# Kernel tuning notes

Measured on AMD Instinct MI355X. Metric: run time of the kernel, lower is better.

Reference implementation:

```python
import jax, jax.numpy as jnp
import numpy as np

CIN = 128
COUT = 128
B = 8192
N_DIAG = 17
LENS = [9 - abs(i - 8) for i in range(N_DIAG)]  # [1,2,...,9,...,2,1]


def setup_inputs() -> dict:
    key = jax.random.key(0)
    ks = jax.random.split(key, 2 + N_DIAG)
    d = {
        "weights": jax.random.normal(ks[0], (N_DIAG, COUT, CIN), jnp.float32),
        "bias": jax.random.normal(ks[1], (N_DIAG, COUT), jnp.float32),
    }
    for i, L in enumerate(LENS):
        d[f"x{i}"] = jax.random.normal(ks[2 + i], (B, L, CIN), jnp.float32)
    return d


def _diag_idx(i):
    # board positions (r, c) on anti-diagonal r + c == i of a 9x9 board
    rs = np.arange(max(0, i - 8), min(8, i) + 1)
    cs = i - rs
    return rs, cs


def _forward(weights, bias, xs):
    b = xs[0].shape[0]
    out = jnp.zeros((b, 9, 9, weights.shape[1]), xs[0].dtype)
    for i, x in enumerate(xs):
        # per-diagonal linear transform: (B, L_i, Cin) @ (Cout, Cin)^T + bias
        y = jnp.einsum('blc,oc->blo', x, weights[i]) + bias[i]
        rs, cs = _diag_idx(i)  # static numpy indices -> jit-friendly scatter
        out = out.at[:, rs, cs, :].set(y)
    return out


def reference(weights, bias, x0, x1, x2, x3, x4, x5, x6, x7, x8, x9, x10, x11,
              x12, x13, x14, x15, x16):
    xs = (x0, x1, x2, x3, x4, x5, x6, x7, x8, x9, x10, x11, x12, x13, x14,
          x15, x16)
    return _forward(weights, bias, xs)
```

## Files before the change

### kernel.cpp

```cpp
#include <hip/hip_runtime.h>
#include <hip/hip_bf16.h>

typedef __attribute__((ext_vector_type(8))) short short8;
typedef __attribute__((ext_vector_type(4))) float f32x4;
typedef __attribute__((ext_vector_type(4))) unsigned int u32x4;

struct XPtrs { const float* p[17]; };
struct Bases { int v[18]; };

#define CPB 8

__device__ __forceinline__ unsigned short f2bf(float f) {
  unsigned u = __float_as_uint(f);
  return (unsigned short)((u + 0x7fffu + ((u >> 16) & 1u)) >> 16);
}

__global__ __launch_bounds__(1024) void convert_w_kernel(
    const float* __restrict__ W, unsigned short* __restrict__ ws) {
  const int tid = blockIdx.x * 1024 + threadIdx.x;
  const int d  = tid >> 11;
  const int s2 = tid & 2047;
  const int sg = s2 >> 7;
  const int n  = s2 & 127;
  const float* src = W + ((size_t)d * 128 + n) * 128 + sg * 8;
  float4 a = *(const float4*)(src);
  float4 b = *(const float4*)(src + 4);
  unsigned u0 = (unsigned)f2bf(a.x) | ((unsigned)f2bf(a.y) << 16);
  unsigned u1 = (unsigned)f2bf(a.z) | ((unsigned)f2bf(a.w) << 16);
  unsigned u2 = (unsigned)f2bf(b.x) | ((unsigned)f2bf(b.y) << 16);
  unsigned u3 = (unsigned)f2bf(b.z) | ((unsigned)f2bf(b.w) << 16);
  *(uint4*)(ws + (size_t)tid * 8) = make_uint4(u0, u1, u2, u3);
}

__device__ __forceinline__ unsigned pack_bf2(float lo, float hi) {
  unsigned rl = __float_as_uint(lo) + 0x8000u;
  unsigned rh = __float_as_uint(hi) + 0x8000u;
  return __builtin_amdgcn_perm(rh, rl, 0x07060302u);
}

__device__ __forceinline__ void issue_unit_loads(
    const float* __restrict__ x, int u, int wave, int lr, int lg,
    float4 (&pf)[8]) {
  const float* xr = x + ((size_t)(u * 64 + wave * 16 + lr)) * 128 + lg * 8;
#pragma unroll
  for (int s = 0; s < 4; ++s) {
    pf[2 * s]     = *(const float4*)(xr + s * 32);
    pf[2 * s + 1] = *(const float4*)(xr + s * 32 + 4);
  }
}

__device__ __forceinline__ void convert_unit(const float4 (&pf)[8],
                                             short8 (&xf)[4]) {
#pragma unroll
  for (int s = 0; s < 4; ++s) {
    float4 a0 = pf[2 * s], a1 = pf[2 * s + 1];
    u32x4 w;
    w.x = pack_bf2(a0.x, a0.y);
    w.y = pack_bf2(a0.z, a0.w);
    w.z = pack_bf2(a1.x, a1.y);
    w.w = pack_bf2(a1.z, a1.w);
    xf[s] = __builtin_bit_cast(short8, w);
  }
}

__global__ __launch_bounds__(256) void diag_linear_kernel(
    XPtrs xp, Bases bb, const unsigned short* __restrict__ wsrc,
    const float* __restrict__ bias, float* __restrict__ out) {
  const int bid = blockIdx.x;
  int d = 0;
#pragma unroll
  for (int i = 1; i < 17; ++i) d += (bid >= bb.v[i]) ? 1 : 0;
  const int L = 9 - ((d < 8) ? (8 - d) : (d - 8));
  const int start = (d > 8) ? (d - 8) : 0;
  const float* __restrict__ x = xp.p[d];
  const int u0 = (bid - bb.v[d]) * CPB;

  const int t = threadIdx.x;
  const int lane = t & 63;
  const int wave = t >> 6;
  const int lr = lane & 15;
  const int lg = lane >> 4;

  __shared__ unsigned short wlds[2048 * 8];
  __shared__ float blds[128];

  {
    const unsigned short* gw = wsrc + (size_t)d * 16384;
    typedef const __attribute__((address_space(1))) unsigned int* gas_u32;
    typedef __attribute__((address_space(3))) unsigned int* las_u32;
#pragma unroll
    for (int r = 0; r < 8; ++r) {
      const int slotbase = (wave * 8 + r) * 64;
      __builtin_amdgcn_global_load_lds(
          (gas_u32)(const void*)(gw + (size_t)(slotbase + lane) * 8),
          (las_u32)(void*)(wlds + (size_t)slotbase * 8),
          16, 0, 0);
    }
    if (t < 32) {
      __builtin_amdgcn_global_load_lds(
          (gas_u32)(const void*)(bias + d * 128 + t * 4),
          (las_u32)(void*)(blds), 16, 0, 0);
    }
  }

  float4 pA[8], pB[8];
  issue_unit_loads(x, u0,     wave, lr, lg, pA);
  issue_unit_loads(x, u0 + 1, wave, lr, lg, pB);

  __syncthreads();

  const int npair = CPB / 2;
#pragma unroll
  for (int k = 0; k < npair; ++k) {
#pragma unroll
    for (int ph = 0; ph < 2; ++ph) {
      const int u = u0 + 2 * k + ph;

      short8 xf[4];
      if (ph == 0) convert_unit(pA, xf);
      else         convert_unit(pB, xf);

      if (k + 1 < npair) {
        if (ph == 0) issue_unit_loads(x, u + 2, wave, lr, lg, pA);
        else         issue_unit_loads(x, u + 2, wave, lr, lg, pB);
      }

      f32x4 acc[8];
#pragma unroll
      for (int nb = 0; nb < 8; ++nb)
        acc[nb] = *(const f32x4*)&blds[nb * 16 + lg * 4];

#pragma unroll
      for (int s = 0; s < 4; ++s) {
#pragma unroll
        for (int nb = 0; nb < 8; ++nb) {
          short8 wf = *(const short8*)
              &wlds[(size_t)((s * 4 + lg) * 128 + nb * 16 + lr) * 8];
          acc[nb] = __builtin_amdgcn_mfma_f32_16x16x32_bf16(wf, xf[s], acc[nb], 0, 0, 0);
        }
      }

      const int f = u * 64 + wave * 16 + lr;
      const unsigned b = (unsigned)f / (unsigned)L;
      const int l = f - (int)b * L;
      float* orow = out + (size_t)b * 10368 + (size_t)(start * 8 + d) * 128
                    + (size_t)l * 1024 + lg * 4;
#pragma unroll
      for (int nb = 0; nb < 8; ++nb)
        *(f32x4*)(orow + nb * 16) = acc[nb];
    }
  }
}

extern "C" void kernel_launch(void* const* d_in, const int* in_sizes, int n_in,
                              void* d_out, int out_size, void* d_ws, size_t ws_size,
                              hipStream_t stream) {
  const float* W = (const float*)d_in[0];
  const float* bias = (const float*)d_in[1];
  XPtrs xp;
  for (int i = 0; i < 17; ++i) xp.p[i] = (const float*)d_in[2 + i];
  float* out = (float*)d_out;
  unsigned short* ws = (unsigned short*)d_ws;

  Bases bb;
  int base = 0;
  for (int i = 0; i < 17; ++i) {
    bb.v[i] = base;
    int L = 9 - ((i < 8) ? (8 - i) : (i - 8));
    base += (128 * L) / CPB;
  }
  bb.v[17] = base;

  convert_w_kernel<<<34, 1024, 0, stream>>>(W, ws);
  diag_linear_kernel<<<base, 256, 0, stream>>>(xp, bb, ws, bias, out);
}
```

Measured before the change: 161.1 us.

## Fuse weight bf16 conversion into main kernel and single-buffer x prefetch

Removes the separate weight-conversion kernel launch. Each block now loads its diagonal's fp32 weights itself, rounds them to bf16 with round-to-nearest-even and writes them to LDS. The main loop changes from a double-buffered, fully unrolled pair loop to a single-buffered loop that is not unrolled. That cuts register pressure but exposes more load latency. Every block now redundantly reads 64KB of fp32 weights instead of 32KB of bf16, with a synchronous load path before the barrier.

```diff
diff --git a/kernel.cpp b/kernel.cpp
--- a/kernel.cpp
+++ b/kernel.cpp
@@ -10,26 +10,12 @@
 
 #define CPB 8
 
-__device__ __forceinline__ unsigned short f2bf(float f) {
-  unsigned u = __float_as_uint(f);
-  return (unsigned short)((u + 0x7fffu + ((u >> 16) & 1u)) >> 16);
-}
-
-__global__ __launch_bounds__(1024) void convert_w_kernel(
-    const float* __restrict__ W, unsigned short* __restrict__ ws) {
-  const int tid = blockIdx.x * 1024 + threadIdx.x;
-  const int d  = tid >> 11;
-  const int s2 = tid & 2047;
-  const int sg = s2 >> 7;
-  const int n  = s2 & 127;
-  const float* src = W + ((size_t)d * 128 + n) * 128 + sg * 8;
-  float4 a = *(const float4*)(src);
-  float4 b = *(const float4*)(src + 4);
-  unsigned u0 = (unsigned)f2bf(a.x) | ((unsigned)f2bf(a.y) << 16);
-  unsigned u1 = (unsigned)f2bf(a.z) | ((unsigned)f2bf(a.w) << 16);
-  unsigned u2 = (unsigned)f2bf(b.x) | ((unsigned)f2bf(b.y) << 16);
-  unsigned u3 = (unsigned)f2bf(b.z) | ((unsigned)f2bf(b.w) << 16);
-  *(uint4*)(ws + (size_t)tid * 8) = make_uint4(u0, u1, u2, u3);
+__device__ __forceinline__ unsigned pack_bf2_rne(float lo, float hi) {
+  unsigned ul = __float_as_uint(lo);
+  unsigned uh = __float_as_uint(hi);
+  ul += 0x7fffu + ((ul >> 16) & 1u);
+  uh += 0x7fffu + ((uh >> 16) & 1u);
+  return __builtin_amdgcn_perm(uh, ul, 0x07060302u);
 }
 
 __device__ __forceinline__ unsigned pack_bf2(float lo, float hi) {
@@ -64,7 +50,7 @@
 }
 
 __global__ __launch_bounds__(256) void diag_linear_kernel(
-    XPtrs xp, Bases bb, const unsigned short* __restrict__ wsrc,
+    XPtrs xp, Bases bb, const float* __restrict__ W,
     const float* __restrict__ bias, float* __restrict__ out) {
   const int bid = blockIdx.x;
   int d = 0;
@@ -85,70 +71,68 @@
   __shared__ float blds[128];
 
   {
-    const unsigned short* gw = wsrc + (size_t)d * 16384;
-    typedef const __attribute__((address_space(1))) unsigned int* gas_u32;
-    typedef __attribute__((address_space(3))) unsigned int* las_u32;
+    const int n = t & 127;
+    const int kh = t >> 7;
+    const float* wrow = W + (size_t)d * 16384 + (size_t)n * 128 + kh * 64;
 #pragma unroll
-    for (int r = 0; r < 8; ++r) {
-      const int slotbase = (wave * 8 + r) * 64;
-      __builtin_amdgcn_global_load_lds(
-          (gas_u32)(const void*)(gw + (size_t)(slotbase + lane) * 8),
-          (las_u32)(void*)(wlds + (size_t)slotbase * 8),
-          16, 0, 0);
+    for (int itw = 0; itw < 8; ++itw) {
+      float4 a = *(const float4*)(wrow + itw * 8);
+      float4 b = *(const float4*)(wrow + itw * 8 + 4);
+      u32x4 v;
+      v.x = pack_bf2_rne(a.x, a.y);
+      v.y = pack_bf2_rne(a.z, a.w);
+      v.z = pack_bf2_rne(b.x, b.y);
+      v.w = pack_bf2_rne(b.z, b.w);
+      const int slot = (kh * 8 + itw) * 128 + n;
+      *(u32x4*)&wlds[(size_t)slot * 8] = v;
     }
     if (t < 32) {
+      typedef const __attribute__((address_space(1))) unsigned int* gas_u32;
+      typedef __attribute__((address_space(3))) unsigned int* las_u32;
       __builtin_amdgcn_global_load_lds(
           (gas_u32)(const void*)(bias + d * 128 + t * 4),
           (las_u32)(void*)(blds), 16, 0, 0);
     }
   }
 
-  float4 pA[8], pB[8];
-  issue_unit_loads(x, u0,     wave, lr, lg, pA);
-  issue_unit_loads(x, u0 + 1, wave, lr, lg, pB);
+  float4 pf[8];
+  issue_unit_loads(x, u0, wave, lr, lg, pf);
 
   __syncthreads();
 
-  const int npair = CPB / 2;
+#pragma unroll 1
+  for (int it = 0; it < CPB; ++it) {
+    const int u = u0 + it;
+
+    short8 xf[4];
+    convert_unit(pf, xf);
+
+    if (it + 1 < CPB)
+      issue_unit_loads(x, u + 1, wave, lr, lg, pf);
+
+    f32x4 acc[8];
 #pragma unroll
-  for (int k = 0; k < npair; ++k) {
-#pragma unroll
-    for (int ph = 0; ph < 2; ++ph) {
-      const int u = u0 + 2 * k + ph;
-
-      short8 xf[4];
-      if (ph == 0) convert_unit(pA, xf);
-      else         convert_unit(pB, xf);
-
-      if (k + 1 < npair) {
-        if (ph == 0) issue_unit_loads(x, u + 2, wave, lr, lg, pA);
-        else         issue_unit_loads(x, u + 2, wave, lr, lg, pB);
-      }
-
-      f32x4 acc[8];
-#pragma unroll
-      for (int nb = 0; nb < 8; ++nb)
-        acc[nb] = *(const f32x4*)&blds[nb * 16 + lg * 4];
+    for (int nb = 0; nb < 8; ++nb)
+      acc[nb] = *(const f32x4*)&blds[nb * 16 + lg * 4];
 
 #pragma unroll
-      for (int s = 0; s < 4; ++s) {
+    for (int s = 0; s < 4; ++s) {
 #pragma unroll
-        for (int nb = 0; nb < 8; ++nb) {
-          short8 wf = *(const short8*)
-              &wlds[(size_t)((s * 4 + lg) * 128 + nb * 16 + lr) * 8];
-          acc[nb] = __builtin_amdgcn_mfma_f32_16x16x32_bf16(wf, xf[s], acc[nb], 0, 0, 0);
-        }
+      for (int nb = 0; nb < 8; ++nb) {
+        short8 wf = *(const short8*)
+            &wlds[(size_t)((s * 4 + lg) * 128 + nb * 16 + lr) * 8];
+        acc[nb] = __builtin_amdgcn_mfma_f32_16x16x32_bf16(wf, xf[s], acc[nb], 0, 0, 0);
       }
+    }
 
-      const int f = u * 64 + wave * 16 + lr;
-      const unsigned b = (unsigned)f / (unsigned)L;
-      const int l = f - (int)b * L;
-      float* orow = out + (size_t)b * 10368 + (size_t)(start * 8 + d) * 128
-                    + (size_t)l * 1024 + lg * 4;
+    const int f = u * 64 + wave * 16 + lr;
+    const unsigned b = (unsigned)f / (unsigned)L;
+    const int l = f - (int)b * L;
+    float* orow = out + (size_t)b * 10368 + (size_t)(start * 8 + d) * 128
+                  + (size_t)l * 1024 + lg * 4;
 #pragma unroll
-      for (int nb = 0; nb < 8; ++nb)
-        *(f32x4*)(orow + nb * 16) = acc[nb];
-    }
+    for (int nb = 0; nb < 8; ++nb)
+      *(f32x4*)(orow + nb * 16) = acc[nb];
   }
 }
 
@@ -160,17 +144,15 @@
   XPtrs xp;
   for (int i = 0; i < 17; ++i) xp.p[i] = (const float*)d_in[2 + i];
   float* out = (float*)d_out;
-  unsigned short* ws = (unsigned short*)d_ws;
 
   Bases bb;
   int base = 0;
   for (int i = 0; i < 17; ++i) {
     bb.v[i] = base;
     int L = 9 - ((i < 8) ? (8 - i) : (i - 8));
-    base += (128 * L) / CPB;
+    base += 16 * L;
   }
   bb.v[17] = base;
 
-  convert_w_kernel<<<34, 1024, 0, stream>>>(W, ws);
-  diag_linear_kernel<<<base, 256, 0, stream>>>(xp, bb, ws, bias, out);
+  diag_linear_kernel<<<base, 256, 0, stream>>>(xp, bb, W, bias, out);
 }
```

After: 163.7 us. Within noise of the previous version (+1.6%).

## Halve units per block, reorder MFMA loop per output block, stop unrolling

Applied to the files above, without the earlier changes.

Cuts the units each block processes from 8 to 4, which doubles the grid size. The inner compute is reordered so each 16-column output block runs its 4 chained MFMAs and is stored right away. This drops the eight live accumulator vectors to one, lowering register pressure and raising occupancy. In exchange the MFMAs are now serially dependent, there are more per-block weight loads into LDS, and the outer loop is no longer unrolled.

```diff
diff --git a/kernel.cpp b/kernel.cpp
--- a/kernel.cpp
+++ b/kernel.cpp
@@ -8,7 +8,7 @@
 struct XPtrs { const float* p[17]; };
 struct Bases { int v[18]; };
 
-#define CPB 8
+#define CPB 4
 
 __device__ __forceinline__ unsigned short f2bf(float f) {
   unsigned u = __float_as_uint(f);
@@ -63,6 +63,28 @@
   }
 }
 
+__device__ __forceinline__ void compute_store_unit(
+    const short8 (&xf)[4], const unsigned short* __restrict__ wlds,
+    const float* __restrict__ blds, int u, int wave, int lr, int lg,
+    int L, int start, int d, float* __restrict__ out) {
+  const int f = u * 64 + wave * 16 + lr;
+  const unsigned b = (unsigned)f / (unsigned)L;
+  const int l = f - (int)b * L;
+  float* orow = out + (size_t)b * 10368 + (size_t)(start * 8 + d) * 128
+                + (size_t)l * 1024 + lg * 4;
+#pragma unroll
+  for (int nb = 0; nb < 8; ++nb) {
+    f32x4 acc = *(const f32x4*)&blds[nb * 16 + lg * 4];
+#pragma unroll
+    for (int s = 0; s < 4; ++s) {
+      short8 wf = *(const short8*)
+          &wlds[(size_t)((s * 4 + lg) * 128 + nb * 16 + lr) * 8];
+      acc = __builtin_amdgcn_mfma_f32_16x16x32_bf16(wf, xf[s], acc, 0, 0, 0);
+    }
+    *(f32x4*)(orow + nb * 16) = acc;
+  }
+}
+
 __global__ __launch_bounds__(256) void diag_linear_kernel(
     XPtrs xp, Bases bb, const unsigned short* __restrict__ wsrc,
     const float* __restrict__ bias, float* __restrict__ out) {
@@ -109,45 +131,24 @@
 
   __syncthreads();
 
-  const int npair = CPB / 2;
-#pragma unroll
-  for (int k = 0; k < npair; ++k) {
-#pragma unroll
-    for (int ph = 0; ph < 2; ++ph) {
-      const int u = u0 + 2 * k + ph;
+#pragma unroll 1
+  for (int k = 0; k < CPB / 2; ++k) {
+    const int uA = u0 + 2 * k;
 
+    {
       short8 xf[4];
-      if (ph == 0) convert_unit(pA, xf);
-      else         convert_unit(pB, xf);
+      convert_unit(pA, xf);
+      if (2 * k + 2 < CPB)
+        issue_unit_loads(x, uA + 2, wave, lr, lg, pA);
+      compute_store_unit(xf, wlds, blds, uA, wave, lr, lg, L, start, d, out);
+    }
 
-      if (k + 1 < npair) {
-        if (ph == 0) issue_unit_loads(x, u + 2, wave, lr, lg, pA);
-        else         issue_unit_loads(x, u + 2, wave, lr, lg, pB);
-      }
-
-      f32x4 acc[8];
-#pragma unroll
-      for (int nb = 0; nb < 8; ++nb)
-        acc[nb] = *(const f32x4*)&blds[nb * 16 + lg * 4];
-
-#pragma unroll
-      for (int s = 0; s < 4; ++s) {
-#pragma unroll
-        for (int nb = 0; nb < 8; ++nb) {
-          short8 wf = *(const short8*)
-              &wlds[(size_t)((s * 4 + lg) * 128 + nb * 16 + lr) * 8];
-          acc[nb] = __builtin_amdgcn_mfma_f32_16x16x32_bf16(wf, xf[s], acc[nb], 0, 0, 0);
-        }
-      }
-
-      const int f = u * 64 + wave * 16 + lr;
-      const unsigned b = (unsigned)f / (unsigned)L;
-      const int l = f - (int)b * L;
-      float* orow = out + (size_t)b * 10368 + (size_t)(start * 8 + d) * 128
-                    + (size_t)l * 1024 + lg * 4;
-#pragma unroll
-      for (int nb = 0; nb < 8; ++nb)
-        *(f32x4*)(orow + nb * 16) = acc[nb];
+    {
+      short8 xf[4];
+      convert_unit(pB, xf);
+      if (2 * k + 3 < CPB)
+        issue_unit_loads(x, uA + 3, wave, lr, lg, pB);
+      compute_store_unit(xf, wlds, blds, uA + 1, wave, lr, lg, L, start, d, out);
     }
   }
 }
```

Measured after the change: 153.1 us. 5.0% less time.
